# Kernel optimization log

Measured on AMD Instinct MI355X. Metric: run time of the kernel, lower is better.

The kernel has to match this reference:

```python
import jax, jax.numpy as jnp
import numpy as np

DIM = 1024
NUM_HEADS = 16
HEAD_DIM = DIM // NUM_HEADS
B, S, E = 4, 8192, 2000


def setup_inputs() -> dict:
    key = jax.random.key(0)
    ks = jax.random.split(key, 16)
    sd = 0.02
    inp = {
        "x": jax.random.normal(ks[0], (B, S, DIM), dtype=jnp.float32),
        "src_indices": jax.random.randint(ks[1], (E,), 0, S),
        "dst_indices": jax.random.randint(ks[2], (E,), 0, S),
        # linear weights stored [in, out] (applied as x @ W + b)
        "Wq": jax.random.normal(ks[3], (DIM, DIM), jnp.float32) * sd,
        "bq": jnp.zeros((DIM,), jnp.float32),
        "Wk": jax.random.normal(ks[4], (DIM, DIM), jnp.float32) * sd,
        "bk": jnp.zeros((DIM,), jnp.float32),
        "Wv": jax.random.normal(ks[5], (DIM, DIM), jnp.float32) * sd,
        "bv": jnp.zeros((DIM,), jnp.float32),
        "Wo": jax.random.normal(ks[6], (DIM, DIM), jnp.float32) * sd,
        "bo": jnp.zeros((DIM,), jnp.float32),
        "edge_weight": jax.random.normal(ks[7], (1, NUM_HEADS, 1), jnp.float32),
        "W1": jax.random.normal(ks[8], (2 * HEAD_DIM, HEAD_DIM), jnp.float32) * sd,
        "b1": jnp.zeros((HEAD_DIM,), jnp.float32),
        "W2": jax.random.normal(ks[9], (HEAD_DIM, 1), jnp.float32) * sd,
        "b2": jnp.zeros((1,), jnp.float32),
    }
    return inp


def reference(x, src_indices, dst_indices, Wq, bq, Wk, bk, Wv, bv, Wo, bo,
              edge_weight, W1, b1, W2, b2):
    Bs, Sl, D = x.shape
    H, hd = NUM_HEADS, HEAD_DIM
    scale = hd ** -0.5

    def heads(t):  # [B,S,D] -> [B,H,S,hd]
        return t.reshape(Bs, Sl, H, hd).transpose(0, 2, 1, 3)

    q = heads(x @ Wq + bq)
    k = heads(x @ Wk + bk)
    v = heads(x @ Wv + bv)

    q_src = jnp.take(q, src_indices, axis=2)   # [B,H,E,hd]
    k_dst = jnp.take(k, dst_indices, axis=2)   # [B,H,E,hd]
    v_dst = jnp.take(v, dst_indices, axis=2)   # [B,H,E,hd]

    ef = jnp.concatenate([q_src, k_dst], axis=-1)          # [B,H,E,2hd]
    h = jax.nn.gelu(ef @ W1 + b1, approximate=False)       # [B,H,E,hd]
    scores = (h @ W2 + b2) * scale                         # [B,H,E,1]
    attn = jax.nn.softmax(scores, axis=2)                  # softmax over all edges
    attn = attn * edge_weight[..., None]                   # [1,H,1,1] broadcast

    weighted = attn * v_dst                                # [B,H,E,hd]
    out = jnp.zeros((Bs, H, Sl, hd), x.dtype).at[:, :, src_indices, :].add(weighted)

    final = out.transpose(0, 2, 1, 3).reshape(Bs, Sl, D)
    return final @ Wo + bo
```

## Files before the change

### kernel.cpp

```cpp
#include <hip/hip_runtime.h>
#include <hip/hip_bf16.h>
#include <math.h>

#define DIMK 1024
#define NH 16
#define HD 64
#define BB 4
#define SS 8192
#define EPAD 136
#define NT 96

typedef __attribute__((ext_vector_type(8))) short bf16x8;
typedef __attribute__((ext_vector_type(8))) unsigned short ushort8;
typedef __attribute__((ext_vector_type(4))) unsigned short us4;
typedef __attribute__((ext_vector_type(4))) float f32x4;

#define MFMA16(a, b, c) __builtin_amdgcn_mfma_f32_16x16x32_bf16((a), (b), (c), 0, 0, 0)

__device__ __forceinline__ unsigned short f32_to_bf16_rne(float f) {
  unsigned int u = __float_as_uint(f);
  u = (u + 0x7fffu + ((u >> 16) & 1u)) >> 16;
  return (unsigned short)u;
}
__device__ __forceinline__ float bf16_bits_to_f32(unsigned short b) {
  return __uint_as_float(((unsigned int)b) << 16);
}
__device__ __forceinline__ void gload16(const void* g, void* l) {
  __builtin_amdgcn_global_load_lds((const __attribute__((address_space(1))) void*)g,
                                   (__attribute__((address_space(3))) void*)l, 16, 0, 0);
}

__global__ __launch_bounds__(256) void fill_out_kernel(const float4* __restrict__ bo4,
                                                       float4* __restrict__ out, int total4) {
  for (int i = blockIdx.x * 256 + threadIdx.x; i < total4; i += gridDim.x * 256)
    out[i] = bo4[i & 255];
}

__global__ __launch_bounds__(256) void prep_w4(
    const float* __restrict__ Wq, const float* __restrict__ Wk,
    const float* __restrict__ Wv, const float* __restrict__ Wo,
    unsigned short* __restrict__ Bq, unsigned short* __restrict__ Bkv,
    unsigned short* __restrict__ Bo) {
  const float* W;
  unsigned short* Bpan;
  int pnoff;
  switch (blockIdx.z) {
    case 0: W = Wq; Bpan = Bq; pnoff = 0; break;
    case 1: W = Wk; Bpan = Bkv; pnoff = 0; break;
    case 2: W = Wv; Bpan = Bkv; pnoff = 8; break;
    default: W = Wo; Bpan = Bo; pnoff = 0; break;
  }
  __shared__ float st[64][65];
  const int bk = blockIdx.x * 64, bn = blockIdx.y * 64;
  const int t = threadIdx.x;
  const int lr = t >> 4, lc = (t & 15) * 4;
#pragma unroll
  for (int i = 0; i < 4; i++) {
    int k = lr + i * 16;
    float4 v = *(const float4*)(W + (size_t)(bk + k) * DIMK + bn + lc);
    st[k][lc] = v.x; st[k][lc + 1] = v.y; st[k][lc + 2] = v.z; st[k][lc + 3] = v.w;
  }
  __syncthreads();
  const int ktile = (bk + lc) >> 5, c = lc & 31;
#pragma unroll
  for (int i = 0; i < 4; i++) {
    const int nl = lr + i * 16;
    const int n = bn + nl;
    const int r = n & 127, pn = (n >> 7) + pnoff;
    const int q = (c >> 3) ^ ((r >> 1) & 3);
    const size_t byteoff = (size_t)r * 64 + q * 16 + (c & 7) * 2;
    us4 hv, lv;
#pragma unroll
    for (int j = 0; j < 4; j++) {
      float v = st[lc + j][nl];
      unsigned short hb = f32_to_bf16_rne(v);
      hv[j] = hb;
      lv[j] = f32_to_bf16_rne(v - bf16_bits_to_f32(hb));
    }
    char* base = (char*)Bpan;
    *(us4*)(base + (((size_t)pn * 64 + ktile) << 13) + byteoff) = hv;
    *(us4*)(base + (((size_t)pn * 64 + 32 + ktile) << 13) + byteoff) = lv;
  }
}

__global__ __launch_bounds__(256) void prep_w1(const float* __restrict__ W1,
                                               unsigned short* __restrict__ W1Th,
                                               unsigned short* __restrict__ W1Tl) {
  for (int idx = threadIdx.x; idx < 128 * 64; idx += 256) {
    int k = idx >> 6, n = idx & 63;
    float v = W1[idx];
    unsigned short hb = f32_to_bf16_rne(v);
    W1Th[n * 128 + k] = hb;
    W1Tl[n * 128 + k] = f32_to_bf16_rne(v - bf16_bits_to_f32(hb));
  }
}

__global__ __launch_bounds__(256) void prep_a(const float* __restrict__ X,
                                              const int* __restrict__ gidx,
                                              unsigned short* __restrict__ Apan, int M, int E) {
  const int row = blockIdx.x;
  const int r = row & 255, mt = row >> 8;
  const int c0 = threadIdx.x * 4;
  const int kt = c0 >> 5, c = c0 & 31;
  const int q = (c >> 3) ^ ((r >> 1) & 3);
  const size_t byteoff = (size_t)r * 64 + q * 16 + (c & 7) * 2;
  char* base = (char*)Apan;
  us4 hv = (us4){0, 0, 0, 0}, lv = (us4){0, 0, 0, 0};
  if (row < M) {
    const float* sr;
    if (gidx) {
      int b = row / E, e = row - b * E;
      sr = X + ((size_t)b * SS + gidx[e]) * DIMK;
    } else {
      sr = X + (size_t)row * DIMK;
    }
    float4 v = *(const float4*)(sr + c0);
    float vv[4] = {v.x, v.y, v.z, v.w};
#pragma unroll
    for (int i = 0; i < 4; i++) {
      unsigned short hb = f32_to_bf16_rne(vv[i]);
      hv[i] = hb;
      lv[i] = f32_to_bf16_rne(vv[i] - bf16_bits_to_f32(hb));
    }
  }
  *(us4*)(base + (((size_t)(mt * 64 + kt)) << 14) + byteoff) = hv;
  *(us4*)(base + (((size_t)(mt * 64 + 32 + kt)) << 14) + byteoff) = lv;
}

__global__ __launch_bounds__(1024) void first_occ(const int* __restrict__ src,
                                                  int* __restrict__ fidx,
                                                  int* __restrict__ mark, int E) {
  __shared__ int tbl[SS];
  for (int i = threadIdx.x; i < SS; i += 1024) tbl[i] = 0x7fffffff;
  __syncthreads();
  for (int e = threadIdx.x; e < E; e += 1024) atomicMin(&tbl[src[e]], e);
  __syncthreads();
  for (int e = threadIdx.x; e < E; e += 1024) mark[e] = 0;
  __syncthreads();
  for (int e = threadIdx.x; e < E; e += 1024) {
    int f = tbl[src[e]];
    fidx[e] = f;
    if (f != e) mark[f] = 1;
  }
}

template <int BN, int MODE>
__global__ __launch_bounds__(512, 2) void gemm8(
    const unsigned short* __restrict__ Apan, const unsigned short* __restrict__ Bpan,
    const float* __restrict__ bias, const float* __restrict__ bias2,
    float* __restrict__ out, int ldc, int nty,
    const int* __restrict__ fidx, const int* __restrict__ srci, int M, int E) {
  constexpr int NF = BN / 64;
  constexpr int BTILE = BN * 32;
  constexpr int VM2 = (BN == 256) ? 8 : 6;
  constexpr int VM1 = (BN == 256) ? 4 : 3;
  __shared__ unsigned short ldsA[4][8192];
  __shared__ unsigned short ldsB[4][BTILE];

  const int tid = threadIdx.x, lane = tid & 63, wv = tid >> 6;
  const int wr = wv >> 2, wc = wv & 3;

  const int w = (blockIdx.x & 7) * ((int)gridDim.x >> 3) + ((int)blockIdx.x >> 3);
  const int mt = w / nty, nt_ = w - mt * nty;
  const int m0 = mt * 256, n0 = nt_ * BN;

  const int rr = lane & 15, lq = lane >> 4;
  const int swz = (rr >> 1) & 3;
  const int aoff = (wr * 128 + rr) * 32 + ((lq ^ swz) << 3);
  const int boff = (wc * (BN / 4) + rr) * 32 + ((lq ^ swz) << 3);

  const char* Apb = (const char*)Apan + ((size_t)(mt * 64) << 14);
  const char* Bpb = (const char*)Bpan;
  const int stoff = wv * 1024 + lane * 16;

  f32x4 acc[8][NF];
#pragma unroll
  for (int i = 0; i < 8; i++)
#pragma unroll
    for (int j = 0; j < NF; j++) acc[i][j] = (f32x4){0.f, 0.f, 0.f, 0.f};

  auto stageA = [&](int kt) {
    const int apk = kt < 64 ? kt : kt - 64;
    const char* s = Apb + ((size_t)apk << 14) + stoff;
    gload16(s, &ldsA[kt & 3][wv * 512]);
    gload16(s + 8192, &ldsA[kt & 3][wv * 512 + 4096]);
  };
  auto stageB = [&](int kt) {
    const int bpk = kt < 32 ? kt : kt - 32;
    if (BN == 256) {
      const char* s0 = Bpb + (((size_t)(2 * nt_) * 64 + bpk) << 13) + stoff;
      const char* s1 = Bpb + (((size_t)(2 * nt_ + 1) * 64 + bpk) << 13) + stoff;
      gload16(s0, &ldsB[kt & 3][wv * 512]);
      gload16(s1, &ldsB[kt & 3][wv * 512 + 4096]);
    } else {
      const char* s0 = Bpb + (((size_t)nt_ * 64 + bpk) << 13) + stoff;
      gload16(s0, &ldsB[kt & 3][wv * 512]);
    }
  };
  auto readFrags = [&](int kt, bf16x8* fa, bf16x8* fb) {
    const unsigned short* Al = ldsA[kt & 3];
    const unsigned short* Bl = ldsB[kt & 3];
#pragma unroll
    for (int nf = 0; nf < NF; ++nf) fb[nf] = *(const bf16x8*)(Bl + boff + nf * 512);
#pragma unroll
    for (int mf = 0; mf < 8; ++mf) fa[mf] = *(const bf16x8*)(Al + aoff + mf * 512);
  };
  auto doMFMA = [&](bf16x8* fa, bf16x8* fb) {
    __builtin_amdgcn_s_setprio(1);
#pragma unroll
    for (int mf = 0; mf < 8; ++mf)
#pragma unroll
      for (int nf = 0; nf < NF; ++nf) acc[mf][nf] = MFMA16(fa[mf], fb[nf], acc[mf][nf]);
    __builtin_amdgcn_s_setprio(0);
  };

  bf16x8 faA[8], fbA[NF], faB[8], fbB[NF];

  stageA(0); stageB(0);
  stageA(1); stageB(1);
  stageA(2); stageB(2);
  asm volatile("s_waitcnt vmcnt(%0)" ::"i"(VM2) : "memory");
  __builtin_amdgcn_sched_barrier(0);
  __builtin_amdgcn_s_barrier();
  readFrags(0, faA, fbA);

  for (int kt = 0; kt < NT; kt += 2) {
    if (kt + 3 < NT) { stageA(kt + 3); stageB(kt + 3); }
    asm volatile("s_waitcnt lgkmcnt(0)" ::: "memory");
    if (kt + 3 < NT) {
      asm volatile("s_waitcnt vmcnt(%0)" ::"i"(VM2) : "memory");
    } else if (kt + 2 < NT) {
      asm volatile("s_waitcnt vmcnt(%0)" ::"i"(VM1) : "memory");
    } else {
      asm volatile("s_waitcnt vmcnt(0)" ::: "memory");
    }
    __builtin_amdgcn_sched_barrier(0);
    __builtin_amdgcn_s_barrier();
    readFrags(kt + 1, faB, fbB);
    doMFMA(faA, fbA);

    if (kt + 4 < NT) { stageA(kt + 4); stageB(kt + 4); }
    asm volatile("s_waitcnt lgkmcnt(0)" ::: "memory");
    if (kt + 4 < NT) {
      asm volatile("s_waitcnt vmcnt(%0)" ::"i"(VM2) : "memory");
    } else if (kt + 3 < NT) {
      asm volatile("s_waitcnt vmcnt(%0)" ::"i"(VM1) : "memory");
    } else {
      asm volatile("s_waitcnt vmcnt(0)" ::: "memory");
    }
    __builtin_amdgcn_sched_barrier(0);
    __builtin_amdgcn_s_barrier();
    if (kt + 2 < NT) readFrags(kt + 2, faA, fbA);
    doMFMA(faB, fbB);
  }

  const int cq = lane >> 4, cr = lane & 15;
#pragma unroll
  for (int nf = 0; nf < NF; ++nf) {
    const int col = n0 + wc * (BN / 4) + nf * 16 + cr;
    const float bv = (MODE == 0 && bias2 != nullptr && col >= DIMK) ? bias2[col - DIMK]
                                                                    : bias[col & (DIMK - 1)];
#pragma unroll
    for (int mf = 0; mf < 8; ++mf) {
#pragma unroll
      for (int r = 0; r < 4; ++r) {
        const int mrow = m0 + wr * 128 + mf * 16 + cq * 4 + r;
        if (mrow >= M) continue;
        if (MODE == 0) {
          out[(size_t)mrow * ldc + col] = acc[mf][nf][r] + bv;
        } else {
          int b = mrow / E, e = mrow - b * E;
          if (fidx[e] == e) {
            int orow = b * SS + srci[e];
            out[(size_t)orow * ldc + col] = acc[mf][nf][r] + bv;
          }
        }
      }
    }
  }
}

__global__ __launch_bounds__(256) void edge_scores_mfma(
    const float* __restrict__ qs, const float* __restrict__ kd, int ldk,
    const unsigned short* __restrict__ W1Th, const unsigned short* __restrict__ W1Tl,
    const float* __restrict__ b1, const float* __restrict__ W2,
    const float* __restrict__ b2, float* __restrict__ scores, int E, int CH) {
  __shared__ unsigned short W1h[64][EPAD], W1l[64][EPAD];
  __shared__ unsigned short EFh[4][16][EPAD], EFl[4][16][EPAD];
  const int tid = threadIdx.x, lane = tid & 63, w = tid >> 6;
  const int bh = blockIdx.x / CH, ch = blockIdx.x - bh * CH;
  const int b = bh >> 4, h = bh & 15;

  for (int idx = tid; idx < 64 * 16; idx += 256) {
    int n = idx >> 4, g = (idx & 15) * 8;
    *(ushort8*)&W1h[n][g] = *(const ushort8*)(W1Th + n * 128 + g);
    *(ushort8*)&W1l[n][g] = *(const ushort8*)(W1Tl + n * 128 + g);
  }
  __syncthreads();

  const int etile = ch * 4 + w;
  const int e0 = etile * 16;
  if (e0 >= E) return;

  const int r = lane >> 2, c0 = (lane & 3) * 16;
  {
    const int er = (e0 + r < E) ? e0 + r : E - 1;
    const float* qrow = qs + ((size_t)(b * E + er)) * DIMK + h * HD + c0;
    const float* krow = kd + ((size_t)(b * E + er)) * (size_t)ldk + h * HD + c0;
    float qv[16], kvv[16];
#pragma unroll
    for (int i = 0; i < 4; i++) {
      *(float4*)&qv[i * 4] = *(const float4*)(qrow + i * 4);
      *(float4*)&kvv[i * 4] = *(const float4*)(krow + i * 4);
    }
    ushort8 qh[2], ql[2], kh[2], kl[2];
#pragma unroll
    for (int g = 0; g < 2; g++)
#pragma unroll
      for (int i = 0; i < 8; i++) {
        float v = qv[g * 8 + i];
        unsigned short hb = f32_to_bf16_rne(v);
        qh[g][i] = hb;
        ql[g][i] = f32_to_bf16_rne(v - bf16_bits_to_f32(hb));
        float v2 = kvv[g * 8 + i];
        unsigned short hb2 = f32_to_bf16_rne(v2);
        kh[g][i] = hb2;
        kl[g][i] = f32_to_bf16_rne(v2 - bf16_bits_to_f32(hb2));
      }
    *(ushort8*)&EFh[w][r][c0] = qh[0];
    *(ushort8*)&EFh[w][r][c0 + 8] = qh[1];
    *(ushort8*)&EFl[w][r][c0] = ql[0];
    *(ushort8*)&EFl[w][r][c0 + 8] = ql[1];
    *(ushort8*)&EFh[w][r][64 + c0] = kh[0];
    *(ushort8*)&EFh[w][r][64 + c0 + 8] = kh[1];
    *(ushort8*)&EFl[w][r][64 + c0] = kl[0];
    *(ushort8*)&EFl[w][r][64 + c0 + 8] = kl[1];
  }
  asm volatile("s_waitcnt lgkmcnt(0)" ::: "memory");
  __builtin_amdgcn_sched_barrier(0);

  f32x4 acc[4];
#pragma unroll
  for (int i = 0; i < 4; i++) acc[i] = (f32x4){0.f, 0.f, 0.f, 0.f};

  const int kk = (lane >> 4) * 8, rrl = lane & 15;
#pragma unroll
  for (int ks = 0; ks < 4; ks++) {
    bf16x8 ah = *(bf16x8*)&EFh[w][rrl][ks * 32 + kk];
    bf16x8 al = *(bf16x8*)&EFl[w][rrl][ks * 32 + kk];
#pragma unroll
    for (int nf = 0; nf < 4; nf++) {
      bf16x8 bh_ = *(bf16x8*)&W1h[nf * 16 + rrl][ks * 32 + kk];
      bf16x8 bl_ = *(bf16x8*)&W1l[nf * 16 + rrl][ks * 32 + kk];
      acc[nf] = MFMA16(ah, bh_, acc[nf]);
      acc[nf] = MFMA16(ah, bl_, acc[nf]);
      acc[nf] = MFMA16(al, bh_, acc[nf]);
    }
  }

  const int col_l = lane & 15, rq = lane >> 4;
  float w2v[4], b1v[4];
#pragma unroll
  for (int nf = 0; nf < 4; nf++) {
    w2v[nf] = W2[nf * 16 + col_l];
    b1v[nf] = b1[nf * 16 + col_l];
  }
  float p[4];
#pragma unroll
  for (int rr2 = 0; rr2 < 4; rr2++) {
    float s = 0.f;
#pragma unroll
    for (int nf = 0; nf < 4; nf++) {
      float hv = acc[nf][rr2] + b1v[nf];
      hv = 0.5f * hv * (1.f + erff(hv * 0.70710678118654752f));
      s = fmaf(hv, w2v[nf], s);
    }
    p[rr2] = s;
  }
#pragma unroll
  for (int off = 1; off < 16; off <<= 1)
#pragma unroll
    for (int rr2 = 0; rr2 < 4; rr2++) p[rr2] += __shfl_xor(p[rr2], off, 64);

  if (col_l == 0) {
    const float b2v = b2[0];
#pragma unroll
    for (int rr2 = 0; rr2 < 4; rr2++) {
      int e = e0 + rq * 4 + rr2;
      if (e < E) scores[(size_t)(b * NH + h) * E + e] = (p[rr2] + b2v) * 0.125f;
    }
  }
}

__global__ __launch_bounds__(256) void softmax_ew(float* __restrict__ scores,
                                                  const float* __restrict__ ew, int E) {
  const int row = blockIdx.x;
  const int h = row & (NH - 1);
  float* s = scores + (size_t)row * E;
  const int tid = threadIdx.x, lane = tid & 63, w = tid >> 6;
  __shared__ float red[4];

  float vals[8];
  float mx = -1e30f;
#pragma unroll
  for (int i = 0; i < 8; i++) {
    int j = tid + i * 256;
    vals[i] = (j < E) ? s[j] : -1e30f;
    mx = fmaxf(mx, vals[i]);
  }
#pragma unroll
  for (int off = 32; off; off >>= 1) mx = fmaxf(mx, __shfl_xor(mx, off, 64));
  if (lane == 0) red[w] = mx;
  __syncthreads();
  mx = fmaxf(fmaxf(red[0], red[1]), fmaxf(red[2], red[3]));
  __syncthreads();

  float sum = 0.f;
#pragma unroll
  for (int i = 0; i < 8; i++) {
    vals[i] = __expf(vals[i] - mx);
    if (tid + i * 256 < E) sum += vals[i];
  }
#pragma unroll
  for (int off = 32; off; off >>= 1) sum += __shfl_xor(sum, off, 64);
  if (lane == 0) red[w] = sum;
  __syncthreads();
  sum = red[0] + red[1] + red[2] + red[3];

  const float scaleout = ew[h] / sum;
#pragma unroll
  for (int i = 0; i < 8; i++) {
    int j = tid + i * 256;
    if (j < E) s[j] = vals[i] * scaleout;
  }
}

__global__ __launch_bounds__(256) void weight_split(
    const float* __restrict__ vd, int ldv, const float* __restrict__ attn,
    float* __restrict__ wrow, unsigned short* __restrict__ Apan, int M, int E) {
  const int row = blockIdx.x;
  const int r = row & 255, mt = row >> 8;
  const int c0 = threadIdx.x * 4;
  const int kt = c0 >> 5, c = c0 & 31;
  const int q = (c >> 3) ^ ((r >> 1) & 3);
  const size_t byteoff = (size_t)r * 64 + q * 16 + (c & 7) * 2;
  char* base = (char*)Apan;
  us4 hv = (us4){0, 0, 0, 0}, lv = (us4){0, 0, 0, 0};
  if (row < M) {
    const int b = row / E, e = row - b * E;
    const float a = attn[(size_t)(b * NH + (c0 >> 6)) * E + e];
    float4 v = *(const float4*)(vd + (size_t)row * ldv + c0);
    v.x *= a; v.y *= a; v.z *= a; v.w *= a;
    *(float4*)(wrow + (size_t)row * DIMK + c0) = v;
    float vv[4] = {v.x, v.y, v.z, v.w};
#pragma unroll
    for (int i = 0; i < 4; i++) {
      unsigned short hb = f32_to_bf16_rne(vv[i]);
      hv[i] = hb;
      lv[i] = f32_to_bf16_rne(vv[i] - bf16_bits_to_f32(hb));
    }
  }
  *(us4*)(base + (((size_t)(mt * 64 + kt)) << 14) + byteoff) = hv;
  *(us4*)(base + (((size_t)(mt * 64 + 32 + kt)) << 14) + byteoff) = lv;
}

__global__ __launch_bounds__(256) void dup_add(const int* __restrict__ f,
                                               float* __restrict__ wrow, int E) {
  const int e = blockIdx.x;
  const int fe = f[e];
  if (fe == e) return;
  const int d = threadIdx.x * 4;
#pragma unroll
  for (int b = 0; b < BB; b++) {
    const float4 v = *(const float4*)(wrow + (size_t)(b * E + e) * DIMK + d);
    float* dst = wrow + (size_t)(b * E + fe) * DIMK + d;
    atomicAdd(dst + 0, v.x);
    atomicAdd(dst + 1, v.y);
    atomicAdd(dst + 2, v.z);
    atomicAdd(dst + 3, v.w);
  }
}

__global__ __launch_bounds__(256) void dup_fix(const int* __restrict__ fidx,
                                               const int* __restrict__ mark,
                                               const float* __restrict__ wrow,
                                               unsigned short* __restrict__ Apan, int E) {
  const int e = blockIdx.x;
  if (fidx[e] != e || !mark[e]) return;
  const int c0 = threadIdx.x * 4;
  const int kt = c0 >> 5, c = c0 & 31;
  char* base = (char*)Apan;
  for (int b = 0; b < BB; b++) {
    const int row = b * E + e;
    const int r = row & 255, mt = row >> 8;
    const int q = (c >> 3) ^ ((r >> 1) & 3);
    const size_t byteoff = (size_t)r * 64 + q * 16 + (c & 7) * 2;
    float4 v = *(const float4*)(wrow + (size_t)row * DIMK + c0);
    float vv[4] = {v.x, v.y, v.z, v.w};
    us4 hv, lv;
#pragma unroll
    for (int i = 0; i < 4; i++) {
      unsigned short hb = f32_to_bf16_rne(vv[i]);
      hv[i] = hb;
      lv[i] = f32_to_bf16_rne(vv[i] - bf16_bits_to_f32(hb));
    }
    *(us4*)(base + (((size_t)(mt * 64 + kt)) << 14) + byteoff) = hv;
    *(us4*)(base + (((size_t)(mt * 64 + 32 + kt)) << 14) + byteoff) = lv;
  }
}

extern "C" void kernel_launch(void* const* d_in, const int* in_sizes, int n_in,
                              void* d_out, int out_size, void* d_ws, size_t ws_size,
                              hipStream_t stream) {
  const float* x = (const float*)d_in[0];
  const int* src = (const int*)d_in[1];
  const int* dst = (const int*)d_in[2];
  const float* Wq = (const float*)d_in[3];
  const float* bq = (const float*)d_in[4];
  const float* Wk = (const float*)d_in[5];
  const float* bk = (const float*)d_in[6];
  const float* Wv = (const float*)d_in[7];
  const float* bv = (const float*)d_in[8];
  const float* Wo = (const float*)d_in[9];
  const float* bo = (const float*)d_in[10];
  const float* ew = (const float*)d_in[11];
  const float* W1 = (const float*)d_in[12];
  const float* b1 = (const float*)d_in[13];
  const float* W2 = (const float*)d_in[14];
  const float* b2 = (const float*)d_in[15];
  float* out = (float*)d_out;

  const int E = in_sizes[1];
  const int M = BB * E;
  const int gx = (M + 255) / 256;
  const int Mpad = gx * 256;

  char* w = (char*)d_ws;
  float* qs = (float*)w; w += (size_t)M * DIMK * 4;
  float* kv = (float*)w; w += (size_t)M * 2048 * 4;
  float* sc = (float*)w; w += (size_t)BB * NH * E * 4;
  int* fidx = (int*)w; w += (((size_t)E * 4) + 255) & ~(size_t)255;
  int* mark = (int*)w; w += (((size_t)E * 4) + 255) & ~(size_t)255;
  unsigned short* W1Th = (unsigned short*)w; w += 64 * 128 * 2;
  unsigned short* W1Tl = (unsigned short*)w; w += 64 * 128 * 2;
  unsigned short* Bq = (unsigned short*)w; w += (size_t)8 * 64 * 8192;
  unsigned short* Bkv = (unsigned short*)w; w += (size_t)16 * 64 * 8192;
  unsigned short* Bo = (unsigned short*)w; w += (size_t)8 * 64 * 8192;
  unsigned short* Apan = (unsigned short*)w; w += (size_t)gx * 64 * 16384;

  float* wrow = qs;

  const int total4 = BB * SS * (DIMK / 4);
  fill_out_kernel<<<2048, 256, 0, stream>>>((const float4*)bo, (float4*)out, total4);

  prep_w4<<<dim3(16, 16, 4), 256, 0, stream>>>(Wq, Wk, Wv, Wo, Bq, Bkv, Bo);
  prep_w1<<<1, 256, 0, stream>>>(W1, W1Th, W1Tl);

  first_occ<<<1, 1024, 0, stream>>>(src, fidx, mark, E);

  prep_a<<<Mpad, 256, 0, stream>>>(x, src, Apan, M, E);
  gemm8<128, 0><<<gx * 8, 512, 0, stream>>>(Apan, Bq, bq, nullptr, qs, DIMK, 8,
                                            nullptr, nullptr, M, E);

  prep_a<<<Mpad, 256, 0, stream>>>(x, dst, Apan, M, E);
  gemm8<256, 0><<<gx * 8, 512, 0, stream>>>(Apan, Bkv, bk, bv, kv, 2048, 8,
                                            nullptr, nullptr, M, E);

  const int etiles = (E + 15) / 16;
  const int CH = (etiles + 3) / 4;
  edge_scores_mfma<<<BB * NH * CH, 256, 0, stream>>>(qs, kv, 2048, W1Th, W1Tl, b1, W2, b2,
                                                     sc, E, CH);
  softmax_ew<<<BB * NH, 256, 0, stream>>>(sc, ew, E);

  weight_split<<<Mpad, 256, 0, stream>>>(kv + 1024, 2048, sc, wrow, Apan, M, E);
  dup_add<<<E, 256, 0, stream>>>(fidx, wrow, E);
  dup_fix<<<E, 256, 0, stream>>>(fidx, mark, wrow, Apan, E);

  gemm8<128, 1><<<gx * 8, 512, 0, stream>>>(Apan, Bo, bo, nullptr, out, DIMK, 8,
                                            fidx, src, M, E);
}
```

Measured before the change: 386.6 us.

## Restructure split-bf16 GEMM loop to load hi/lo tiles together, double-buffered

The GEMM previously walked 96 K-steps over a concatenated hi/lo panel (hi*hi, lo*hi, hi*lo passes) with a 4-stage LDS ring. It now runs 32 K-steps, staging the hi and lo parts of A and B together into double-buffered LDS and issuing the three MFMA passes per step from shared fragments, which cuts A/B-hi LDS reads and the barrier count. In exchange the prefetch depth drops from three stages to one, which exposes more global-load latency. LDS use per block changes, which may affect the two-blocks-per-CU occupancy.

After: 350.1 us. 9.4% less time.

```diff
diff --git a/kernel.cpp b/kernel.cpp
--- a/kernel.cpp
+++ b/kernel.cpp
@@ -8,7 +8,7 @@
 #define BB 4
 #define SS 8192
 #define EPAD 136
-#define NT 96
+#define NKT 32
 
 typedef __attribute__((ext_vector_type(8))) short bf16x8;
 typedef __attribute__((ext_vector_type(8))) unsigned short ushort8;
@@ -151,11 +151,11 @@
     float* __restrict__ out, int ldc, int nty,
     const int* __restrict__ fidx, const int* __restrict__ srci, int M, int E) {
   constexpr int NF = BN / 64;
-  constexpr int BTILE = BN * 32;
-  constexpr int VM2 = (BN == 256) ? 8 : 6;
-  constexpr int VM1 = (BN == 256) ? 4 : 3;
-  __shared__ unsigned short ldsA[4][8192];
-  __shared__ unsigned short ldsB[4][BTILE];
+  constexpr int BT = BN * 32;
+  __shared__ unsigned short ldsAh[2][8192];
+  __shared__ unsigned short ldsAl[2][8192];
+  __shared__ unsigned short ldsBh[2][BT];
+  __shared__ unsigned short ldsBl[2][BT];
 
   const int tid = threadIdx.x, lane = tid & 63, wv = tid >> 6;
   const int wr = wv >> 2, wc = wv & 3;
@@ -179,79 +179,86 @@
 #pragma unroll
     for (int j = 0; j < NF; j++) acc[i][j] = (f32x4){0.f, 0.f, 0.f, 0.f};
 
-  auto stageA = [&](int kt) {
-    const int apk = kt < 64 ? kt : kt - 64;
-    const char* s = Apb + ((size_t)apk << 14) + stoff;
-    gload16(s, &ldsA[kt & 3][wv * 512]);
-    gload16(s + 8192, &ldsA[kt & 3][wv * 512 + 4096]);
+  auto stage = [&](int kt, int buf) {
+    const char* sAh = Apb + ((size_t)kt << 14) + stoff;
+    const char* sAl = Apb + ((size_t)(32 + kt) << 14) + stoff;
+    gload16(sAh, &ldsAh[buf][wv * 512]);
+    gload16(sAh + 8192, &ldsAh[buf][wv * 512 + 4096]);
+    gload16(sAl, &ldsAl[buf][wv * 512]);
+    gload16(sAl + 8192, &ldsAl[buf][wv * 512 + 4096]);
+    if (BN == 256) {
+      const char* sB0h = Bpb + (((size_t)(2 * nt_) * 64 + kt) << 13) + stoff;
+      const char* sB1h = Bpb + (((size_t)(2 * nt_ + 1) * 64 + kt) << 13) + stoff;
+      const char* sB0l = Bpb + (((size_t)(2 * nt_) * 64 + 32 + kt) << 13) + stoff;
+      const char* sB1l = Bpb + (((size_t)(2 * nt_ + 1) * 64 + 32 + kt) << 13) + stoff;
+      gload16(sB0h, &ldsBh[buf][wv * 512]);
+      gload16(sB1h, &ldsBh[buf][wv * 512 + 4096]);
+      gload16(sB0l, &ldsBl[buf][wv * 512]);
+      gload16(sB1l, &ldsBl[buf][wv * 512 + 4096]);
+    } else {
+      const char* sBh = Bpb + (((size_t)nt_ * 64 + kt) << 13) + stoff;
+      const char* sBl = Bpb + (((size_t)nt_ * 64 + 32 + kt) << 13) + stoff;
+      gload16(sBh, &ldsBh[buf][wv * 512]);
+      gload16(sBl, &ldsBl[buf][wv * 512]);
+    }
   };
-  auto stageB = [&](int kt) {
-    const int bpk = kt < 32 ? kt : kt - 32;
-    if (BN == 256) {
-      const char* s0 = Bpb + (((size_t)(2 * nt_) * 64 + bpk) << 13) + stoff;
-      const char* s1 = Bpb + (((size_t)(2 * nt_ + 1) * 64 + bpk) << 13) + stoff;
-      gload16(s0, &ldsB[kt & 3][wv * 512]);
-      gload16(s1, &ldsB[kt & 3][wv * 512 + 4096]);
-    } else {
-      const char* s0 = Bpb + (((size_t)nt_ * 64 + bpk) << 13) + stoff;
-      gload16(s0, &ldsB[kt & 3][wv * 512]);
-    }
-  };
-  auto readFrags = [&](int kt, bf16x8* fa, bf16x8* fb) {
-    const unsigned short* Al = ldsA[kt & 3];
-    const unsigned short* Bl = ldsB[kt & 3];
-#pragma unroll
-    for (int nf = 0; nf < NF; ++nf) fb[nf] = *(const bf16x8*)(Bl + boff + nf * 512);
-#pragma unroll
-    for (int mf = 0; mf < 8; ++mf) fa[mf] = *(const bf16x8*)(Al + aoff + mf * 512);
-  };
-  auto doMFMA = [&](bf16x8* fa, bf16x8* fb) {
-    __builtin_amdgcn_s_setprio(1);
-#pragma unroll
-    for (int mf = 0; mf < 8; ++mf)
-#pragma unroll
-      for (int nf = 0; nf < NF; ++nf) acc[mf][nf] = MFMA16(fa[mf], fb[nf], acc[mf][nf]);
-    __builtin_amdgcn_s_setprio(0);
-  };
-
-  bf16x8 faA[8], fbA[NF], faB[8], fbB[NF];
-
-  stageA(0); stageB(0);
-  stageA(1); stageB(1);
-  stageA(2); stageB(2);
-  asm volatile("s_waitcnt vmcnt(%0)" ::"i"(VM2) : "memory");
+
+  stage(0, 0);
+  asm volatile("s_waitcnt vmcnt(0)" ::: "memory");
   __builtin_amdgcn_sched_barrier(0);
   __builtin_amdgcn_s_barrier();
-  readFrags(0, faA, fbA);
-
-  for (int kt = 0; kt < NT; kt += 2) {
-    if (kt + 3 < NT) { stageA(kt + 3); stageB(kt + 3); }
+
+  for (int kt = 0; kt < NKT; ++kt) {
+    const int buf = kt & 1;
+    const unsigned short* Ah = ldsAh[buf];
+    const unsigned short* Al = ldsAl[buf];
+    const unsigned short* Bh = ldsBh[buf];
+    const unsigned short* Bl = ldsBl[buf];
+
+    bf16x8 fbh[NF], fah[8], fal[8], fbl[NF];
+#pragma unroll
+    for (int nf = 0; nf < NF; ++nf) fbh[nf] = *(const bf16x8*)(Bh + boff + nf * 512);
+#pragma unroll
+    for (int mf = 0; mf < 8; ++mf) fah[mf] = *(const bf16x8*)(Ah + aoff + mf * 512);
+#pragma unroll
+    for (int mf = 0; mf < 8; ++mf) fal[mf] = *(const bf16x8*)(Al + aoff + mf * 512);
+
+    if (kt + 1 < NKT) stage(kt + 1, buf ^ 1);
+
+    asm volatile("s_waitcnt lgkmcnt(8)" ::: "memory");
+    __builtin_amdgcn_sched_barrier(0);
+    __builtin_amdgcn_s_setprio(1);
+#pragma unroll
+    for (int mf = 0; mf < 8; ++mf)
+#pragma unroll
+      for (int nf = 0; nf < NF; ++nf) acc[mf][nf] = MFMA16(fah[mf], fbh[nf], acc[mf][nf]);
+    __builtin_amdgcn_s_setprio(0);
+
     asm volatile("s_waitcnt lgkmcnt(0)" ::: "memory");
-    if (kt + 3 < NT) {
-      asm volatile("s_waitcnt vmcnt(%0)" ::"i"(VM2) : "memory");
-    } else if (kt + 2 < NT) {
-      asm volatile("s_waitcnt vmcnt(%0)" ::"i"(VM1) : "memory");
-    } else {
+    __builtin_amdgcn_sched_barrier(0);
+    __builtin_amdgcn_s_setprio(1);
+#pragma unroll
+    for (int mf = 0; mf < 8; ++mf)
+#pragma unroll
+      for (int nf = 0; nf < NF; ++nf) acc[mf][nf] = MFMA16(fal[mf], fbh[nf], acc[mf][nf]);
+    __builtin_amdgcn_s_setprio(0);
+
+#pragma unroll
+    for (int nf = 0; nf < NF; ++nf) fbl[nf] = *(const bf16x8*)(Bl + boff + nf * 512);
+    asm volatile("s_waitcnt lgkmcnt(0)" ::: "memory");
+    __builtin_amdgcn_sched_barrier(0);
+    __builtin_amdgcn_s_setprio(1);
+#pragma unroll
+    for (int mf = 0; mf < 8; ++mf)
+#pragma unroll
+      for (int nf = 0; nf < NF; ++nf) acc[mf][nf] = MFMA16(fah[mf], fbl[nf], acc[mf][nf]);
+    __builtin_amdgcn_s_setprio(0);
+
+    if (kt + 1 < NKT) {
       asm volatile("s_waitcnt vmcnt(0)" ::: "memory");
-    }
-    __builtin_amdgcn_sched_barrier(0);
-    __builtin_amdgcn_s_barrier();
-    readFrags(kt + 1, faB, fbB);
-    doMFMA(faA, fbA);
-
-    if (kt + 4 < NT) { stageA(kt + 4); stageB(kt + 4); }
-    asm volatile("s_waitcnt lgkmcnt(0)" ::: "memory");
-    if (kt + 4 < NT) {
-      asm volatile("s_waitcnt vmcnt(%0)" ::"i"(VM2) : "memory");
-    } else if (kt + 3 < NT) {
-      asm volatile("s_waitcnt vmcnt(%0)" ::"i"(VM1) : "memory");
-    } else {
-      asm volatile("s_waitcnt vmcnt(0)" ::: "memory");
-    }
-    __builtin_amdgcn_sched_barrier(0);
-    __builtin_amdgcn_s_barrier();
-    if (kt + 2 < NT) readFrags(kt + 2, faA, fbA);
-    doMFMA(faB, fbB);
+      __builtin_amdgcn_sched_barrier(0);
+      __builtin_amdgcn_s_barrier();
+    }
   }
 
   const int cq = lane >> 4, cr = lane & 15;
```
